# Kernel tuning notes

Measured on AMD Instinct MI355X. Metric: run time of the kernel, lower is better.

The kernel has to match this reference:

```python
import jax, jax.numpy as jnp
import numpy as np

B, T, HID = 2, 2048, 2048
H, DQ, DV, R = 16, 128, 128, 32
DCQ, DCKV, DCO = 768, 512, 512
EPS = 1e-6
SCALE = DQ ** -0.5


def _rms(x, w):
    xf = x.astype(jnp.float32)
    var = jnp.mean(xf * xf, axis=-1, keepdims=True)
    return w * (xf * jax.lax.rsqrt(var + EPS)).astype(x.dtype)


def _rotate_half(x):
    d = x.shape[-1] // 2
    return jnp.concatenate([-x[..., d:], x[..., :d]], axis=-1)


def setup_inputs() -> dict:
    key = jax.random.key(0)
    ks = jax.random.split(key, 9)
    s = 0.02
    hidden_states = jax.random.normal(ks[0], (B, T, HID), dtype=jnp.float32)
    # RoPE tables: inv_freq over R/2 dims, duplicated (cat(freqs, freqs))
    inv_freq = 1.0 / (10000.0 ** (np.arange(0, R, 2, dtype=np.float32) / R))
    freqs = np.arange(T, dtype=np.float32)[:, None] * inv_freq[None, :]  # [T, R/2]
    emb = np.concatenate([freqs, freqs], axis=-1)  # [T, R]
    cos = jnp.asarray(np.cos(emb))
    sin = jnp.asarray(np.sin(emb))
    return {
        "hidden_states": hidden_states,
        "cos": cos,
        "sin": sin,
        "Wq_shared": jax.random.normal(ks[1], (DCQ, HID), jnp.float32) * s,
        "q_shared_norm_w": jnp.ones((DCQ,), jnp.float32),
        "Wkv_shared": jax.random.normal(ks[2], (DCKV, HID), jnp.float32) * s,
        "kv_shared_norm_w": jnp.ones((DCKV,), jnp.float32),
        "Wq_private": jax.random.normal(ks[3], (H * DQ, DCQ), jnp.float32) * s,
        "Wkv_private": jax.random.normal(ks[4], (H * (DQ + DV), DCKV), jnp.float32) * s,
        "Wg_private": jax.random.normal(ks[5], (H * DV, HID), jnp.float32) * s,
        "Wo_private": jax.random.normal(ks[6], (DCO, H * DV), jnp.float32) * s,
        "o_private_norm_w": jnp.ones((DCO,), jnp.float32),
        "Wo_shared": jax.random.normal(ks[7], (HID, DCO), jnp.float32) * s,
    }


def reference(hidden_states, cos, sin, Wq_shared, q_shared_norm_w, Wkv_shared,
              kv_shared_norm_w, Wq_private, Wkv_private, Wg_private,
              Wo_private, o_private_norm_w, Wo_shared):
    x = hidden_states
    b, t, _ = x.shape
    # shared (latent) projections + RMSNorm
    q_shared = _rms(x @ Wq_shared.T, q_shared_norm_w)    # [B,T,DCQ]
    kv_shared = _rms(x @ Wkv_shared.T, kv_shared_norm_w)  # [B,T,DCKV]
    # private per-head projections
    q = (q_shared @ Wq_private.T).reshape(b, t, H, DQ).transpose(0, 2, 1, 3)
    kv = kv_shared @ Wkv_private.T                        # [B,T,H*(DQ+DV)]
    k_flat, v_flat = jnp.split(kv, 2, axis=-1)            # keys block then values block
    gates = jax.nn.silu(x @ Wg_private.T)                 # [B,T,H*DV]
    v_flat = v_flat * gates
    k = k_flat.reshape(b, t, H, DQ).transpose(0, 2, 1, 3)
    v = v_flat.reshape(b, t, H, DV).transpose(0, 2, 1, 3)
    # partial RoPE on first R dims of each head
    c = cos[None, None]  # [1,1,T,R]
    s = sin[None, None]
    q_rope, q_pass = q[..., :R], q[..., R:]
    k_rope, k_pass = k[..., :R], k[..., R:]
    q = jnp.concatenate([q_rope * c + _rotate_half(q_rope) * s, q_pass], axis=-1)
    k = jnp.concatenate([k_rope * c + _rotate_half(k_rope) * s, k_pass], axis=-1)
    # causal attention
    scores = jnp.einsum('bhqd,bhkd->bhqk', q, k) * SCALE
    causal = jnp.tril(jnp.ones((t, t), dtype=bool))
    scores = jnp.where(causal, scores, jnp.finfo(scores.dtype).min)
    attn = jax.nn.softmax(scores, axis=-1)
    out = jnp.einsum('bhqk,bhkd->bhqd', attn, v)
    out = out.transpose(0, 2, 1, 3).reshape(b, t, H * DV)
    # output subspace: private proj -> norm -> shared proj
    out = _rms(out @ Wo_private.T, o_private_norm_w)
    return out @ Wo_shared.T
```

## Files before the change

kernel.cpp:

```cpp
#include <hip/hip_runtime.h>
#include <stdint.h>

typedef __attribute__((ext_vector_type(8))) short short8;
typedef __attribute__((ext_vector_type(4))) short sh4;
typedef __attribute__((ext_vector_type(4))) float f32x4;

__device__ __forceinline__ float bf2f(unsigned short u) {
  union { unsigned int i; float f; } v; v.i = ((unsigned int)u) << 16; return v.f;
}
__device__ __forceinline__ unsigned short f2bf(float f) {
  union { float f; unsigned int i; } v; v.f = f;
  unsigned int u = v.i;
  return (unsigned short)((u + 0x7fffu + ((u >> 16) & 1u)) >> 16);
}

#define B_SZ 2
#define T_SEQ 2048
#define NH 16
#define DH 128
#define ROPE_R 32
#define SCALE_Q 0.08838834764831845f

template <bool F>
__device__ __forceinline__ short8 ld8(const void* base, size_t idx) {
  if constexpr (F) {
    const float* p = (const float*)base + idx;
    f32x4 a = *(const f32x4*)p;
    f32x4 b = *(const f32x4*)(p + 4);
    short8 r;
    r[0] = (short)f2bf(a[0]); r[1] = (short)f2bf(a[1]);
    r[2] = (short)f2bf(a[2]); r[3] = (short)f2bf(a[3]);
    r[4] = (short)f2bf(b[0]); r[5] = (short)f2bf(b[1]);
    r[6] = (short)f2bf(b[2]); r[7] = (short)f2bf(b[3]);
    return r;
  } else {
    return *(const short8*)((const unsigned short*)base + idx);
  }
}

template <bool AF, bool BF, bool C32>
__global__ __launch_bounds__(256) void gemm_bt(
    const void* __restrict__ Ap, const void* __restrict__ Bp,
    void* __restrict__ Cp, int M, int N, int K) {
  __shared__ unsigned short Al[128][40];
  __shared__ unsigned short Bl[128][40];
  const int tid = threadIdx.x;
  const int lane = tid & 63, w = tid >> 6;
  const int wm = w >> 1, wn = w & 1;
  const int quad = lane >> 4, l16 = lane & 15;
  const int m0 = blockIdx.y * 128, n0 = blockIdx.x * 128;
  f32x4 acc[4][4];
#pragma unroll
  for (int i = 0; i < 4; ++i)
#pragma unroll
    for (int j = 0; j < 4; ++j)
#pragma unroll
      for (int r = 0; r < 4; ++r) acc[i][j][r] = 0.f;

  for (int k0 = 0; k0 < K; k0 += 32) {
    __syncthreads();
#pragma unroll
    for (int p = 0; p < 2; ++p) {
      int v = tid + p * 256;
      int row = v >> 2, kc = (v & 3) * 8;
      *(short8*)&Al[row][kc] = ld8<AF>(Ap, (size_t)(m0 + row) * K + k0 + kc);
      *(short8*)&Bl[row][kc] = ld8<BF>(Bp, (size_t)(n0 + row) * K + k0 + kc);
    }
    __syncthreads();
    short8 a[4];
#pragma unroll
    for (int i = 0; i < 4; ++i)
      a[i] = *(const short8*)&Al[wm * 64 + i * 16 + l16][quad * 8];
#pragma unroll
    for (int j = 0; j < 4; ++j) {
      short8 b = *(const short8*)&Bl[wn * 64 + j * 16 + l16][quad * 8];
#pragma unroll
      for (int i = 0; i < 4; ++i)
        acc[i][j] = __builtin_amdgcn_mfma_f32_16x16x32_bf16(a[i], b, acc[i][j], 0, 0, 0);
    }
  }
#pragma unroll
  for (int i = 0; i < 4; ++i)
#pragma unroll
    for (int j = 0; j < 4; ++j) {
      int row = m0 + wm * 64 + i * 16 + quad * 4;
      int col = n0 + wn * 64 + j * 16 + l16;
#pragma unroll
      for (int r = 0; r < 4; ++r) {
        if constexpr (C32)
          ((float*)Cp)[(size_t)(row + r) * N + col] = acc[i][j][r];
        else
          ((unsigned short*)Cp)[(size_t)(row + r) * N + col] = f2bf(acc[i][j][r]);
      }
    }
}

__device__ __forceinline__ void gload_lds16(const unsigned short* g, unsigned short* l) {
  __builtin_amdgcn_global_load_lds(
      (const __attribute__((address_space(1))) void*)g,
      (__attribute__((address_space(3))) void*)l, 16, 0, 0);
}

template <int BN, bool C32>
__global__ __launch_bounds__(256) void gemm_lds(
    const unsigned short* __restrict__ A, const unsigned short* __restrict__ Bw,
    void* __restrict__ Cp, int M, int N, int K) {
  __shared__ unsigned short Al[128][32];
  __shared__ unsigned short Bl[BN][32];
  const int tid = threadIdx.x;
  const int lane = tid & 63, w = tid >> 6;
  const int wm = w >> 1, wn = w & 1;
  const int quad = lane >> 4, l16 = lane & 15;
  const int m0 = blockIdx.y * 128, n0 = blockIdx.x * BN;
  constexpr int NJ = BN / 32;
  f32x4 acc[4][NJ];
#pragma unroll
  for (int i = 0; i < 4; ++i)
#pragma unroll
    for (int j = 0; j < NJ; ++j)
#pragma unroll
      for (int r = 0; r < 4; ++r) acc[i][j][r] = 0.f;

  for (int k0 = 0; k0 < K; k0 += 32) {
    __syncthreads();
#pragma unroll
    for (int p = 0; p < 2; ++p) {
      int c = w * 128 + p * 64 + lane;
      gload_lds16(A + (size_t)(m0 + (c >> 2)) * K + k0 + (c & 3) * 8,
                  &Al[0][0] + (size_t)(w * 128 + p * 64) * 8);
    }
#pragma unroll
    for (int p = 0; p < BN / 64; ++p) {
      int c = w * BN + p * 64 + lane;
      gload_lds16(Bw + (size_t)(n0 + (c >> 2)) * K + k0 + (c & 3) * 8,
                  &Bl[0][0] + (size_t)(w * BN + p * 64) * 8);
    }
    __syncthreads();
    short8 a[4], b[NJ];
#pragma unroll
    for (int i = 0; i < 4; ++i)
      a[i] = *(const short8*)&Al[wm * 64 + i * 16 + l16][quad * 8];
#pragma unroll
    for (int j = 0; j < NJ; ++j)
      b[j] = *(const short8*)&Bl[wn * (BN / 2) + j * 16 + l16][quad * 8];
#pragma unroll
    for (int j = 0; j < NJ; ++j)
#pragma unroll
      for (int i = 0; i < 4; ++i)
        acc[i][j] = __builtin_amdgcn_mfma_f32_16x16x32_bf16(a[i], b[j], acc[i][j], 0, 0, 0);
  }
#pragma unroll
  for (int i = 0; i < 4; ++i)
#pragma unroll
    for (int j = 0; j < NJ; ++j) {
      int row = m0 + wm * 64 + i * 16 + quad * 4;
      int col = n0 + wn * (BN / 2) + j * 16 + l16;
#pragma unroll
      for (int r = 0; r < 4; ++r) {
        if constexpr (C32)
          ((float*)Cp)[(size_t)(row + r) * N + col] = acc[i][j][r];
        else
          ((unsigned short*)Cp)[(size_t)(row + r) * N + col] = f2bf(acc[i][j][r]);
      }
    }
}

struct CvtArgs {
  const float* src[8];
  unsigned short* dst[8];
  long long n4[8];
};

__global__ __launch_bounds__(256) void cvt_multi(CvtArgs a, long long total4) {
  for (long long g = (long long)blockIdx.x * 256 + threadIdx.x; g < total4;
       g += (long long)gridDim.x * 256) {
    long long r = g;
    int s = 0;
    while (r >= a.n4[s]) { r -= a.n4[s]; ++s; }
    f32x4 v = ((const f32x4*)a.src[s])[r];
    sh4 o;
    o[0] = (short)f2bf(v[0]); o[1] = (short)f2bf(v[1]);
    o[2] = (short)f2bf(v[2]); o[3] = (short)f2bf(v[3]);
    ((sh4*)a.dst[s])[r] = o;
  }
}

__global__ __launch_bounds__(256) void rms_norm_ip(
    unsigned short* __restrict__ x, const float* __restrict__ w, int N) {
  unsigned short* row = x + (size_t)blockIdx.x * N;
  float vals[8];
  int cnt = 0;
  float ss = 0.f;
  for (int j = threadIdx.x; j < N; j += 256) {
    float v = bf2f(row[j]);
    vals[cnt++] = v;
    ss += v * v;
  }
#pragma unroll
  for (int d = 1; d < 64; d <<= 1) ss += __shfl_xor(ss, d);
  __shared__ float ws4[4];
  if ((threadIdx.x & 63) == 0) ws4[threadIdx.x >> 6] = ss;
  __syncthreads();
  float tot = ws4[0] + ws4[1] + ws4[2] + ws4[3];
  float scale = rsqrtf(tot / (float)N + 1e-6f);
  cnt = 0;
  for (int j = threadIdx.x; j < N; j += 256)
    row[j] = f2bf(w[j] * vals[cnt++] * scale);
}

__global__ __launch_bounds__(256) void prep_qk(
    const unsigned short* __restrict__ q_all, const unsigned short* __restrict__ k_all,
    const float* __restrict__ cosb, const float* __restrict__ sinb,
    unsigned short* __restrict__ Q, unsigned short* __restrict__ K) {
  const int bt = blockIdx.x;
  const int b = bt >> 11, t = bt & (T_SEQ - 1);
  const unsigned short* qr = q_all + (size_t)bt * (NH * DH);
  const unsigned short* kr = k_all + (size_t)bt * (NH * DH);
  for (int d = threadIdx.x; d < NH * DH; d += 256) {
    int h = d >> 7, dd = d & 127;
    float qv = bf2f(qr[d]);
    float kv = bf2f(kr[d]);
    if (dd < ROPE_R) {
      float c = cosb[t * ROPE_R + dd];
      float s = sinb[t * ROPE_R + dd];
      float qrot = (dd < 16) ? -bf2f(qr[d + 16]) : bf2f(qr[d - 16]);
      float krot = (dd < 16) ? -bf2f(kr[d + 16]) : bf2f(kr[d - 16]);
      qv = qv * c + qrot * s;
      kv = kv * c + krot * s;
    }
    size_t o = ((size_t)(b * NH + h) * T_SEQ + t) * DH + dd;
    Q[o] = f2bf(qv * SCALE_Q);
    K[o] = f2bf(kv);
  }
}

__global__ __launch_bounds__(256) void prep_vt(
    const unsigned short* __restrict__ v_all, const unsigned short* __restrict__ gates,
    unsigned short* __restrict__ Vt) {
  __shared__ unsigned short tile[64][130];
  const int bh = blockIdx.y, b = bh >> 4, h = bh & 15;
  const int t0 = blockIdx.x * 64;
  for (int idx = threadIdx.x; idx < 64 * 128; idx += 256) {
    int tt = idx >> 7, dd = idx & 127;
    size_t rowbase = (size_t)(b * T_SEQ + t0 + tt);
    float v = bf2f(v_all[rowbase * (NH * DH) + h * DH + dd]);
    float g = bf2f(gates[rowbase * (NH * DH) + h * DH + dd]);
    float sg = g / (1.f + __expf(-g));
    tile[tt][dd] = f2bf(v * sg);
  }
  __syncthreads();
  for (int idx = threadIdx.x; idx < 64 * 128; idx += 256) {
    int dd = idx >> 6, tt = idx & 63;
    Vt[((size_t)bh * DH + dd) * T_SEQ + t0 + tt] = tile[tt][dd];
  }
}

__device__ __forceinline__ void attn_update(
    const unsigned short (*Kl)[132], const unsigned short (*Vl)[68],
    unsigned short (*Pw)[96], const short8* qf, int qt, int kb, bool diag,
    int w, int quad, int l16, f32x4* O, float* m_run, float* l_run) {
  f32x4 sc[4];
  __builtin_amdgcn_s_setprio(1);
#pragma unroll
  for (int jt = 0; jt < 4; ++jt) {
#pragma unroll
    for (int r = 0; r < 4; ++r) sc[jt][r] = 0.f;
#pragma unroll
    for (int kk = 0; kk < 4; ++kk) {
      short8 kf = *(const short8*)&Kl[jt * 16 + l16][kk * 32 + quad * 8];
      sc[jt] = __builtin_amdgcn_mfma_f32_16x16x32_bf16(qf[kk], kf, sc[jt], 0, 0, 0);
    }
  }
  __builtin_amdgcn_s_setprio(0);
  if (diag) {
#pragma unroll
    for (int jt = 0; jt < 4; ++jt) {
      int key = kb + jt * 16 + l16;
#pragma unroll
      for (int r = 0; r < 4; ++r) {
        int row = qt * 64 + w * 16 + quad * 4 + r;
        if (key > row) sc[jt][r] = -1e30f;
      }
    }
  }
  float alpha[4], psum[4];
#pragma unroll
  for (int r = 0; r < 4; ++r) {
    float mx = fmaxf(fmaxf(sc[0][r], sc[1][r]), fmaxf(sc[2][r], sc[3][r]));
    mx = fmaxf(mx, __shfl_xor(mx, 1)); mx = fmaxf(mx, __shfl_xor(mx, 2));
    mx = fmaxf(mx, __shfl_xor(mx, 4)); mx = fmaxf(mx, __shfl_xor(mx, 8));
    float mnew = fmaxf(m_run[r], mx);
    alpha[r] = __expf(m_run[r] - mnew);
    m_run[r] = mnew;
    psum[r] = 0.f;
  }
#pragma unroll
  for (int jt = 0; jt < 4; ++jt)
#pragma unroll
    for (int r = 0; r < 4; ++r) {
      float p = __expf(sc[jt][r] - m_run[r]);
      sc[jt][r] = p;
      psum[r] += p;
    }
#pragma unroll
  for (int r = 0; r < 4; ++r) {
    float s = psum[r];
    s += __shfl_xor(s, 1); s += __shfl_xor(s, 2);
    s += __shfl_xor(s, 4); s += __shfl_xor(s, 8);
    l_run[r] = l_run[r] * alpha[r] + s;
  }
#pragma unroll
  for (int jn = 0; jn < 8; ++jn)
#pragma unroll
    for (int r = 0; r < 4; ++r) O[jn][r] *= alpha[r];
#pragma unroll
  for (int jt = 0; jt < 4; ++jt)
#pragma unroll
    for (int r = 0; r < 4; ++r)
      Pw[quad * 4 + r][jt * 16 + l16] = f2bf(sc[jt][r]);
  short8 pa[2];
#pragma unroll
  for (int kk = 0; kk < 2; ++kk)
    pa[kk] = *(const short8*)&Pw[l16][kk * 32 + quad * 8];
  __builtin_amdgcn_s_setprio(1);
#pragma unroll
  for (int jn = 0; jn < 8; ++jn) {
#pragma unroll
    for (int kk = 0; kk < 2; ++kk) {
      short8 vf = *(const short8*)&Vl[jn * 16 + l16][kk * 32 + quad * 8];
      O[jn] = __builtin_amdgcn_mfma_f32_16x16x32_bf16(pa[kk], vf, O[jn], 0, 0, 0);
    }
  }
  __builtin_amdgcn_s_setprio(0);
}

__global__ __launch_bounds__(256) void flash_attn(
    const unsigned short* __restrict__ Q, const unsigned short* __restrict__ K,
    const unsigned short* __restrict__ Vt, unsigned short* __restrict__ Out) {
  __shared__ unsigned short Kl[64][132];
  __shared__ unsigned short Vl[128][68];
  __shared__ unsigned short P_lds[4][16][96];
  const int l = blockIdx.x;
  const int s = l & 7, qq = l >> 3;
  const int bh = s + 8 * (qq >> 4);
  const int qp = qq & 15;
  const int qa = qp, qb = 31 - qp;
  const int b = bh >> 4, h = bh & 15;
  const int tid = threadIdx.x;
  const int lane = tid & 63, w = tid >> 6;
  const int quad = lane >> 4, l16 = lane & 15;
  const unsigned short* Qb = Q + (size_t)bh * T_SEQ * DH;
  const unsigned short* Kb = K + (size_t)bh * T_SEQ * DH;
  const unsigned short* Vb = Vt + (size_t)bh * DH * T_SEQ;

  short8 qfA[4], qfB[4];
  const int rowA = qa * 64 + w * 16 + l16;
  const int rowB = qb * 64 + w * 16 + l16;
#pragma unroll
  for (int kk = 0; kk < 4; ++kk) {
    qfA[kk] = *(const short8*)&Qb[(size_t)rowA * DH + kk * 32 + quad * 8];
    qfB[kk] = *(const short8*)&Qb[(size_t)rowB * DH + kk * 32 + quad * 8];
  }

  f32x4 OA[8], OB[8];
  float mA[4], lA[4], mB[4], lB[4];
#pragma unroll
  for (int jn = 0; jn < 8; ++jn)
#pragma unroll
    for (int r = 0; r < 4; ++r) { OA[jn][r] = 0.f; OB[jn][r] = 0.f; }
#pragma unroll
  for (int r = 0; r < 4; ++r) { mA[r] = -1e30f; lA[r] = 0.f; mB[r] = -1e30f; lB[r] = 0.f; }

  short8 krg[4], vrg[4];
#pragma unroll
  for (int p = 0; p < 4; ++p) {
    int id = tid + p * 256;
    krg[p] = *(const short8*)&Kb[(size_t)(id >> 4) * DH + (id & 15) * 8];
    vrg[p] = *(const short8*)&Vb[(size_t)(id >> 3) * T_SEQ + (id & 7) * 8];
  }
#pragma unroll
  for (int p = 0; p < 4; ++p) {
    int id = tid + p * 256;
    *(short8*)&Kl[id >> 4][(id & 15) * 8] = krg[p];
    *(short8*)&Vl[id >> 3][(id & 7) * 8] = vrg[p];
  }
  __syncthreads();

  const int last = qb;
  for (int kt = 0; kt <= last; ++kt) {
    const int kb = kt * 64;
    if (kt < last) {
      const int nb = kb + 64;
#pragma unroll
      for (int p = 0; p < 4; ++p) {
        int id = tid + p * 256;
        krg[p] = *(const short8*)&Kb[(size_t)(nb + (id >> 4)) * DH + (id & 15) * 8];
        vrg[p] = *(const short8*)&Vb[(size_t)(id >> 3) * T_SEQ + nb + (id & 7) * 8];
      }
    }
    if (kt <= qa)
      attn_update(Kl, Vl, P_lds[w], qfA, qa, kb, kt == qa, w, quad, l16, OA, mA, lA);
    attn_update(Kl, Vl, P_lds[w], qfB, qb, kb, kt == last, w, quad, l16, OB, mB, lB);
    if (kt < last) {
      __syncthreads();
#pragma unroll
      for (int p = 0; p < 4; ++p) {
        int id = tid + p * 256;
        *(short8*)&Kl[id >> 4][(id & 15) * 8] = krg[p];
        *(short8*)&Vl[id >> 3][(id & 7) * 8] = vrg[p];
      }
      __syncthreads();
    }
  }

#pragma unroll
  for (int jn = 0; jn < 8; ++jn)
#pragma unroll
    for (int r = 0; r < 4; ++r) {
      int ra = qa * 64 + w * 16 + quad * 4 + r;
      int rb = qb * 64 + w * 16 + quad * 4 + r;
      Out[((size_t)(b * T_SEQ) + ra) * (NH * DH) + h * DH + jn * 16 + l16] =
          f2bf(OA[jn][r] / lA[r]);
      Out[((size_t)(b * T_SEQ) + rb) * (NH * DH) + h * DH + jn * 16 + l16] =
          f2bf(OB[jn][r] / lB[r]);
    }
}

extern "C" void kernel_launch(void* const* d_in, const int* in_sizes, int n_in,
                              void* d_out, int out_size, void* d_ws, size_t ws_size,
                              hipStream_t stream) {
  const void*  x     = d_in[0];
  const float* cosb  = (const float*)d_in[1];
  const float* sinb  = (const float*)d_in[2];
  const void*  Wq_s  = d_in[3];
  const float* qs_w  = (const float*)d_in[4];
  const void*  Wkv_s = d_in[5];
  const float* kvs_w = (const float*)d_in[6];
  const void*  Wq_p  = d_in[7];
  const float* Wkv_p = (const float*)d_in[8];
  const void*  Wg_p  = d_in[9];
  const void*  Wo_p  = d_in[10];
  const float* o_w   = (const float*)d_in[11];
  const void*  Wo_s  = d_in[12];
  (void)in_sizes; (void)n_in; (void)out_size;

  const int M = B_SZ * T_SEQ;
  char* ws = (char*)d_ws;
  unsigned short* qs    = (unsigned short*)(ws + 0);
  unsigned short* omid  = qs;
  unsigned short* kvs   = (unsigned short*)(ws + 6291456);
  unsigned short* gates = (unsigned short*)(ws + 10485760);
  unsigned short* k_all = gates;
  unsigned short* v_all = (unsigned short*)(ws + 27262976);
  unsigned short* Qb    = v_all;
  unsigned short* Vt    = (unsigned short*)(ws + 44040192);
  unsigned short* Kb    = (unsigned short*)(ws + 60817408);
  unsigned short* q_all = (unsigned short*)d_out;
  unsigned short* attn  = (unsigned short*)d_out;

  dim3 blk(256);
  const size_t FAST_WS_NEEDED = 119537664;

  if (ws_size >= FAST_WS_NEEDED) {
    unsigned short* xb     = (unsigned short*)(ws + 77594624);
    unsigned short* Wq_s_b = (unsigned short*)(ws + 94371840);
    unsigned short* Wkv_s_b= (unsigned short*)(ws + 97517568);
    unsigned short* Wg_p_b = (unsigned short*)(ws + 99614720);
    unsigned short* Wq_p_b = (unsigned short*)(ws + 108003328);
    unsigned short* Wkv_p_b= (unsigned short*)(ws + 111149056);
    unsigned short* Wo_p_b = (unsigned short*)(ws + 115343360);
    unsigned short* Wo_s_b = (unsigned short*)(ws + 117440512);

    CvtArgs ca;
    ca.src[0] = (const float*)x;    ca.dst[0] = xb;      ca.n4[0] = 2097152;
    ca.src[1] = (const float*)Wq_s; ca.dst[1] = Wq_s_b;  ca.n4[1] = 393216;
    ca.src[2] = (const float*)Wkv_s;ca.dst[2] = Wkv_s_b; ca.n4[2] = 262144;
    ca.src[3] = (const float*)Wg_p; ca.dst[3] = Wg_p_b;  ca.n4[3] = 1048576;
    ca.src[4] = (const float*)Wq_p; ca.dst[4] = Wq_p_b;  ca.n4[4] = 393216;
    ca.src[5] = Wkv_p;              ca.dst[5] = Wkv_p_b; ca.n4[5] = 524288;
    ca.src[6] = (const float*)Wo_p; ca.dst[6] = Wo_p_b;  ca.n4[6] = 262144;
    ca.src[7] = (const float*)Wo_s; ca.dst[7] = Wo_s_b;  ca.n4[7] = 262144;
    long long total4 = 5242880;
    cvt_multi<<<dim3(2048), blk, 0, stream>>>(ca, total4);

    gemm_lds<128, false><<<dim3(768 / 128, M / 128), blk, 0, stream>>>(xb, Wq_s_b, qs, M, 768, 2048);
    gemm_lds<64,  false><<<dim3(512 / 64,  M / 128), blk, 0, stream>>>(xb, Wkv_s_b, kvs, M, 512, 2048);
    gemm_lds<128, false><<<dim3(2048 / 128, M / 128), blk, 0, stream>>>(xb, Wg_p_b, gates, M, 2048, 2048);
    rms_norm_ip<<<M, blk, 0, stream>>>(qs, qs_w, 768);
    rms_norm_ip<<<M, blk, 0, stream>>>(kvs, kvs_w, 512);
    gemm_lds<128, false><<<dim3(2048 / 128, M / 128), blk, 0, stream>>>(qs, Wq_p_b, q_all, M, 2048, 768);
    gemm_lds<128, false><<<dim3(2048 / 128, M / 128), blk, 0, stream>>>(
        kvs, Wkv_p_b + (size_t)2048 * 512, v_all, M, 2048, 512);
    prep_vt<<<dim3(T_SEQ / 64, B_SZ * NH), blk, 0, stream>>>(v_all, gates, Vt);
    gemm_lds<128, false><<<dim3(2048 / 128, M / 128), blk, 0, stream>>>(kvs, Wkv_p_b, k_all, M, 2048, 512);
    prep_qk<<<M, blk, 0, stream>>>(q_all, k_all, cosb, sinb, Qb, Kb);
    flash_attn<<<dim3(512), blk, 0, stream>>>(Qb, Kb, Vt, attn);
    gemm_lds<64,  false><<<dim3(512 / 64, M / 128), blk, 0, stream>>>(attn, Wo_p_b, omid, M, 512, 2048);
    rms_norm_ip<<<M, blk, 0, stream>>>(omid, o_w, 512);
    gemm_lds<128, true><<<dim3(2048 / 128, M / 128), blk, 0, stream>>>(omid, Wo_s_b, d_out, M, 2048, 512);
  } else {
    gemm_bt<true, true, false><<<dim3(768 / 128, M / 128), blk, 0, stream>>>(x, Wq_s, qs, M, 768, 2048);
    gemm_bt<true, true, false><<<dim3(512 / 128, M / 128), blk, 0, stream>>>(x, Wkv_s, kvs, M, 512, 2048);
    gemm_bt<true, true, false><<<dim3(2048 / 128, M / 128), blk, 0, stream>>>(x, Wg_p, gates, M, 2048, 2048);
    rms_norm_ip<<<M, blk, 0, stream>>>(qs, qs_w, 768);
    rms_norm_ip<<<M, blk, 0, stream>>>(kvs, kvs_w, 512);
    gemm_bt<false, true, false><<<dim3(2048 / 128, M / 128), blk, 0, stream>>>(qs, Wq_p, q_all, M, 2048, 768);
    gemm_bt<false, true, false><<<dim3(2048 / 128, M / 128), blk, 0, stream>>>(
        kvs, Wkv_p + (size_t)2048 * 512, v_all, M, 2048, 512);
    prep_vt<<<dim3(T_SEQ / 64, B_SZ * NH), blk, 0, stream>>>(v_all, gates, Vt);
    gemm_bt<false, true, false><<<dim3(2048 / 128, M / 128), blk, 0, stream>>>(kvs, Wkv_p, k_all, M, 2048, 512);
    prep_qk<<<M, blk, 0, stream>>>(q_all, k_all, cosb, sinb, Qb, Kb);
    flash_attn<<<dim3(512), blk, 0, stream>>>(Qb, Kb, Vt, attn);
    gemm_bt<false, true, false><<<dim3(512 / 128, M / 128), blk, 0, stream>>>(attn, Wo_p, omid, M, 512, 2048);
    rms_norm_ip<<<M, blk, 0, stream>>>(omid, o_w, 512);
    gemm_bt<false, true, true><<<dim3(2048 / 128, M / 128), blk, 0, stream>>>(omid, Wo_s, d_out, M, 2048, 512);
  }
}
```

Baseline: 769.3 us.

## Split paired query tiles across separate waves in flash attention with 512-thread blocks

Each flash attention block used 4 waves, and every wave processed both the early (qa) and late (qb) query tiles one after the other. The block now has 8 waves: waves 0-3 own tile qa and waves 4-7 own tile qb, sharing the same K/V LDS tiles, and each thread loads half as much data per stage. This halves per-wave register state and serial work, raising parallelism inside the block. The qa waves go idle once their causal range ends while the qb waves continue, and the larger block may limit how many blocks fit per CU.

```diff
diff --git a/kernel.cpp b/kernel.cpp
--- a/kernel.cpp
+++ b/kernel.cpp
@@ -258,7 +258,7 @@
 __device__ __forceinline__ void attn_update(
     const unsigned short (*Kl)[132], const unsigned short (*Vl)[68],
     unsigned short (*Pw)[96], const short8* qf, int qt, int kb, bool diag,
-    int w, int quad, int l16, f32x4* O, float* m_run, float* l_run) {
+    int wt, int quad, int l16, f32x4* O, float* m_run, float* l_run) {
   f32x4 sc[4];
   __builtin_amdgcn_s_setprio(1);
 #pragma unroll
@@ -278,7 +278,7 @@
       int key = kb + jt * 16 + l16;
 #pragma unroll
       for (int r = 0; r < 4; ++r) {
-        int row = qt * 64 + w * 16 + quad * 4 + r;
+        int row = qt * 64 + wt * 16 + quad * 4 + r;
         if (key > row) sc[jt][r] = -1e30f;
       }
     }
@@ -334,12 +334,12 @@
   __builtin_amdgcn_s_setprio(0);
 }
 
-__global__ __launch_bounds__(256) void flash_attn(
+__global__ __launch_bounds__(512, 4) void flash_attn(
     const unsigned short* __restrict__ Q, const unsigned short* __restrict__ K,
     const unsigned short* __restrict__ Vt, unsigned short* __restrict__ Out) {
   __shared__ unsigned short Kl[64][132];
   __shared__ unsigned short Vl[128][68];
-  __shared__ unsigned short P_lds[4][16][96];
+  __shared__ unsigned short P_lds[8][16][96];
   const int l = blockIdx.x;
   const int s = l & 7, qq = l >> 3;
   const int bh = s + 8 * (qq >> 4);
@@ -348,39 +348,39 @@
   const int b = bh >> 4, h = bh & 15;
   const int tid = threadIdx.x;
   const int lane = tid & 63, w = tid >> 6;
+  const int wt = w & 3;
+  const bool isB = w >= 4;
+  const int myq = isB ? qb : qa;
   const int quad = lane >> 4, l16 = lane & 15;
   const unsigned short* Qb = Q + (size_t)bh * T_SEQ * DH;
   const unsigned short* Kb = K + (size_t)bh * T_SEQ * DH;
   const unsigned short* Vb = Vt + (size_t)bh * DH * T_SEQ;
 
-  short8 qfA[4], qfB[4];
-  const int rowA = qa * 64 + w * 16 + l16;
-  const int rowB = qb * 64 + w * 16 + l16;
-#pragma unroll
-  for (int kk = 0; kk < 4; ++kk) {
-    qfA[kk] = *(const short8*)&Qb[(size_t)rowA * DH + kk * 32 + quad * 8];
-    qfB[kk] = *(const short8*)&Qb[(size_t)rowB * DH + kk * 32 + quad * 8];
-  }
-
-  f32x4 OA[8], OB[8];
-  float mA[4], lA[4], mB[4], lB[4];
+  short8 qf[4];
+  const int qrow = myq * 64 + wt * 16 + l16;
+#pragma unroll
+  for (int kk = 0; kk < 4; ++kk)
+    qf[kk] = *(const short8*)&Qb[(size_t)qrow * DH + kk * 32 + quad * 8];
+
+  f32x4 O[8];
+  float m_run[4], l_run[4];
 #pragma unroll
   for (int jn = 0; jn < 8; ++jn)
 #pragma unroll
-    for (int r = 0; r < 4; ++r) { OA[jn][r] = 0.f; OB[jn][r] = 0.f; }
-#pragma unroll
-  for (int r = 0; r < 4; ++r) { mA[r] = -1e30f; lA[r] = 0.f; mB[r] = -1e30f; lB[r] = 0.f; }
-
-  short8 krg[4], vrg[4];
-#pragma unroll
-  for (int p = 0; p < 4; ++p) {
-    int id = tid + p * 256;
+    for (int r = 0; r < 4; ++r) O[jn][r] = 0.f;
+#pragma unroll
+  for (int r = 0; r < 4; ++r) { m_run[r] = -1e30f; l_run[r] = 0.f; }
+
+  short8 krg[2], vrg[2];
+#pragma unroll
+  for (int p = 0; p < 2; ++p) {
+    int id = tid + p * 512;
     krg[p] = *(const short8*)&Kb[(size_t)(id >> 4) * DH + (id & 15) * 8];
     vrg[p] = *(const short8*)&Vb[(size_t)(id >> 3) * T_SEQ + (id & 7) * 8];
   }
 #pragma unroll
-  for (int p = 0; p < 4; ++p) {
-    int id = tid + p * 256;
+  for (int p = 0; p < 2; ++p) {
+    int id = tid + p * 512;
     *(short8*)&Kl[id >> 4][(id & 15) * 8] = krg[p];
     *(short8*)&Vl[id >> 3][(id & 7) * 8] = vrg[p];
   }
@@ -392,20 +392,20 @@
     if (kt < last) {
       const int nb = kb + 64;
 #pragma unroll
-      for (int p = 0; p < 4; ++p) {
-        int id = tid + p * 256;
+      for (int p = 0; p < 2; ++p) {
+        int id = tid + p * 512;
         krg[p] = *(const short8*)&Kb[(size_t)(nb + (id >> 4)) * DH + (id & 15) * 8];
         vrg[p] = *(const short8*)&Vb[(size_t)(id >> 3) * T_SEQ + nb + (id & 7) * 8];
       }
     }
-    if (kt <= qa)
-      attn_update(Kl, Vl, P_lds[w], qfA, qa, kb, kt == qa, w, quad, l16, OA, mA, lA);
-    attn_update(Kl, Vl, P_lds[w], qfB, qb, kb, kt == last, w, quad, l16, OB, mB, lB);
+    if (isB || kt <= qa)
+      attn_update(Kl, Vl, P_lds[w], qf, myq, kb, kt == (isB ? last : qa),
+                  wt, quad, l16, O, m_run, l_run);
     if (kt < last) {
       __syncthreads();
 #pragma unroll
-      for (int p = 0; p < 4; ++p) {
-        int id = tid + p * 256;
+      for (int p = 0; p < 2; ++p) {
+        int id = tid + p * 512;
         *(short8*)&Kl[id >> 4][(id & 15) * 8] = krg[p];
         *(short8*)&Vl[id >> 3][(id & 7) * 8] = vrg[p];
       }
@@ -417,12 +417,9 @@
   for (int jn = 0; jn < 8; ++jn)
 #pragma unroll
     for (int r = 0; r < 4; ++r) {
-      int ra = qa * 64 + w * 16 + quad * 4 + r;
-      int rb = qb * 64 + w * 16 + quad * 4 + r;
-      Out[((size_t)(b * T_SEQ) + ra) * (NH * DH) + h * DH + jn * 16 + l16] =
-          f2bf(OA[jn][r] / lA[r]);
-      Out[((size_t)(b * T_SEQ) + rb) * (NH * DH) + h * DH + jn * 16 + l16] =
-          f2bf(OB[jn][r] / lB[r]);
+      int rr = myq * 64 + wt * 16 + quad * 4 + r;
+      Out[((size_t)(b * T_SEQ) + rr) * (NH * DH) + h * DH + jn * 16 + l16] =
+          f2bf(O[jn][r] / l_run[r]);
     }
 }
 
@@ -459,6 +456,7 @@
   unsigned short* attn  = (unsigned short*)d_out;
 
   dim3 blk(256);
+  dim3 blk512(512);
   const size_t FAST_WS_NEEDED = 119537664;
 
   if (ws_size >= FAST_WS_NEEDED) {
@@ -494,7 +492,7 @@
     prep_vt<<<dim3(T_SEQ / 64, B_SZ * NH), blk, 0, stream>>>(v_all, gates, Vt);
     gemm_lds<128, false><<<dim3(2048 / 128, M / 128), blk, 0, stream>>>(kvs, Wkv_p_b, k_all, M, 2048, 512);
     prep_qk<<<M, blk, 0, stream>>>(q_all, k_all, cosb, sinb, Qb, Kb);
-    flash_attn<<<dim3(512), blk, 0, stream>>>(Qb, Kb, Vt, attn);
+    flash_attn<<<dim3(512), blk512, 0, stream>>>(Qb, Kb, Vt, attn);
     gemm_lds<64,  false><<<dim3(512 / 64, M / 128), blk, 0, stream>>>(attn, Wo_p_b, omid, M, 512, 2048);
     rms_norm_ip<<<M, blk, 0, stream>>>(omid, o_w, 512);
     gemm_lds<128, true><<<dim3(2048 / 128, M / 128), blk, 0, stream>>>(omid, Wo_s_b, d_out, M, 2048, 512);
@@ -510,7 +508,7 @@
     prep_vt<<<dim3(T_SEQ / 64, B_SZ * NH), blk, 0, stream>>>(v_all, gates, Vt);
     gemm_bt<false, true, false><<<dim3(2048 / 128, M / 128), blk, 0, stream>>>(kvs, Wkv_p, k_all, M, 2048, 512);
     prep_qk<<<M, blk, 0, stream>>>(q_all, k_all, cosb, sinb, Qb, Kb);
-    flash_attn<<<dim3(512), blk, 0, stream>>>(Qb, Kb, Vt, attn);
+    flash_attn<<<dim3(512), blk512, 0, stream>>>(Qb, Kb, Vt, attn);
     gemm_bt<false, true, false><<<dim3(512 / 128, M / 128), blk, 0, stream>>>(attn, Wo_p, omid, M, 512, 2048);
     rms_norm_ip<<<M, blk, 0, stream>>>(omid, o_w, 512);
     gemm_bt<false, true, true><<<dim3(2048 / 128, M / 128), blk, 0, stream>>>(omid, Wo_s, d_out, M, 2048, 512);
```

Result: faster. 729.5 us (-5.2%).
